# Performance work log

Measured on AMD Instinct MI355X. Metric: run time of the kernel, lower is better.

## Reference

```python
import jax, jax.numpy as jnp
import numpy as np

DIM = 1024
HEADS = 16
DIM_HEAD = 64
INNER = HEADS * DIM_HEAD
EPS = 1e-5


def layernorm(x, g, b):
    mu = jnp.mean(x, axis=-1, keepdims=True)
    var = jnp.var(x, axis=-1, keepdims=True)
    return (x - mu) * jax.lax.rsqrt(var + EPS) * g + b


def setup_inputs() -> dict:
    key = jax.random.key(0)
    ks = jax.random.split(key, 16)
    b, n = 2, 2048
    s = 0.02
    inp = {
        "x": jax.random.normal(ks[0], (b, n, DIM), dtype=jnp.float32),
        "ln_g": jnp.ones((DIM,), jnp.float32),
        "ln_b": jnp.zeros((DIM,), jnp.float32),
        "Wq": jax.random.normal(ks[1], (DIM, INNER), jnp.float32) * s,
        "Wkv": jax.random.normal(ks[2], (DIM, 2 * DIM_HEAD), jnp.float32) * s,
        "null_kv": jax.random.normal(ks[3], (2, DIM_HEAD), jnp.float32),
        "null_attn_bias": jax.random.normal(ks[4], (HEADS,), jnp.float32),
        "pb_w0": jax.random.normal(ks[5], (1, DIM), jnp.float32) * s,
        "pb_b0": jnp.zeros((DIM,), jnp.float32),
        "pb_ln0_g": jnp.ones((DIM,), jnp.float32),
        "pb_ln0_b": jnp.zeros((DIM,), jnp.float32),
        "pb_w1": jax.random.normal(ks[6], (DIM, DIM), jnp.float32) * s,
        "pb_b1": jnp.zeros((DIM,), jnp.float32),
        "pb_ln1_g": jnp.ones((DIM,), jnp.float32),
        "pb_ln1_b": jnp.zeros((DIM,), jnp.float32),
        "pb_w2": jax.random.normal(ks[7], (DIM, HEADS), jnp.float32) * s,
        "pb_b2": jnp.zeros((HEADS,), jnp.float32),
        "Wo": jax.random.normal(ks[8], (INNER, DIM), jnp.float32) * s,
        "out_ln_g": jnp.ones((DIM,), jnp.float32),
        "out_ln_b": jnp.zeros((DIM,), jnp.float32),
    }
    return inp


def dynamic_pos_bias(n, pb_w0, pb_b0, pb_ln0_g, pb_ln0_b, pb_w1, pb_b1,
                     pb_ln1_g, pb_ln1_b, pb_w2, pb_b2):
    # pos in [-(n-1), n-1], shape [2n-1, 1]
    pos = jnp.arange(-n + 1, n, dtype=jnp.float32)[:, None]
    h = jax.nn.silu(layernorm(pos @ pb_w0 + pb_b0, pb_ln0_g, pb_ln0_b))
    h = jax.nn.silu(layernorm(h @ pb_w1 + pb_b1, pb_ln1_g, pb_ln1_b))
    h = h @ pb_w2 + pb_b2  # [2n-1, heads]
    i = jnp.arange(n)
    idx = i[:, None] - i[None, :] + (n - 1)  # [n, n]
    bias = h[idx]  # [n, n, heads]
    return jnp.transpose(bias, (2, 0, 1))  # [heads, n, n]


def attention_fwd(x, ln_g, ln_b, Wq, Wkv, null_kv, null_attn_bias,
                  pb_w0, pb_b0, pb_ln0_g, pb_ln0_b, pb_w1, pb_b1,
                  pb_ln1_g, pb_ln1_b, pb_w2, pb_b2, Wo, out_ln_g, out_ln_b):
    b, n, _ = x.shape
    scale = DIM_HEAD ** -0.5
    xn = layernorm(x, ln_g, ln_b)
    q = (xn @ Wq).reshape(b, n, HEADS, DIM_HEAD).transpose(0, 2, 1, 3) * scale  # [b,h,n,d]
    kv = xn @ Wkv  # [b,n,2d]
    k, v = kv[..., :DIM_HEAD], kv[..., DIM_HEAD:]  # single-head MQA kv
    nk = jnp.broadcast_to(null_kv[0], (b, 1, DIM_HEAD))
    nv = jnp.broadcast_to(null_kv[1], (b, 1, DIM_HEAD))
    k = jnp.concatenate([nk, k], axis=1)  # [b, n+1, d]
    v = jnp.concatenate([nv, v], axis=1)
    sim = jnp.einsum('bhid,bjd->bhij', q, k)  # [b,h,n,n+1]
    rel = dynamic_pos_bias(n, pb_w0, pb_b0, pb_ln0_g, pb_ln0_b,
                           pb_w1, pb_b1, pb_ln1_g, pb_ln1_b, pb_w2, pb_b2)
    null_bias = jnp.broadcast_to(null_attn_bias[:, None, None], (HEADS, n, 1))
    attn_bias = jnp.concatenate([null_bias, rel], axis=-1)  # [h, n, n+1]
    sim = sim + attn_bias[None]
    max_neg = -jnp.finfo(sim.dtype).max
    causal_mask = jnp.triu(jnp.ones((n, n + 1), dtype=bool), k=2)
    sim = jnp.where(causal_mask[None, None], max_neg, sim)
    attn = jax.nn.softmax(sim, axis=-1)
    out = jnp.einsum('bhij,bjd->bhid', attn, v)  # [b,h,n,d]
    out = out.transpose(0, 2, 1, 3).reshape(b, n, INNER)
    return layernorm(out @ Wo, out_ln_g, out_ln_b)


def reference(x, ln_g, ln_b, Wq, Wkv, null_kv, null_attn_bias,
              pb_w0, pb_b0, pb_ln0_g, pb_ln0_b, pb_w1, pb_b1,
              pb_ln1_g, pb_ln1_b, pb_w2, pb_b2, Wo, out_ln_g, out_ln_b):
    return attention_fwd(x, ln_g, ln_b, Wq, Wkv, null_kv, null_attn_bias,
                         pb_w0, pb_b0, pb_ln0_g, pb_ln0_b, pb_w1, pb_b1,
                         pb_ln1_g, pb_ln1_b, pb_w2, pb_b2, Wo, out_ln_g, out_ln_b)
```

## Files before the change

### kernel.cpp

```cpp
#include <hip/hip_runtime.h>
#include <hip/hip_bf16.h>
#include <math.h>

#define DIMM   1024
#define NHEADS 16
#define DHEAD  64
#define BATCH  2
#define SEQ    2048
#define NKEYS  (SEQ + 1)
#define NKROWS 2112
#define NKP    2112
#define PBROWS (2 * SEQ - 1)
#define ROWS   (BATCH * SEQ)

using bf16x8 = __attribute__((ext_vector_type(8))) short;
using bf16x4 = __attribute__((ext_vector_type(4))) short;
using f32x4  = __attribute__((ext_vector_type(4))) float;
typedef unsigned int u32;
typedef unsigned short u16;

__device__ __forceinline__ u16 f2bf(float f) {
  __hip_bfloat16 h = __float2bfloat16(f);
  return __builtin_bit_cast(u16, h);
}
__device__ __forceinline__ float bf2f(u16 u) {
  u32 x = ((u32)u) << 16;
  return __builtin_bit_cast(float, x);
}
__device__ __forceinline__ void gl_lds16(const void* g, void* l) {
  __builtin_amdgcn_global_load_lds(
      (const __attribute__((address_space(1))) u32*)g,
      (__attribute__((address_space(3))) u32*)l, 16, 0, 0);
}
__device__ __forceinline__ f32x4 mfma16(bf16x4 a, bf16x4 b, f32x4 c) {
  asm("v_mfma_f32_16x16x16_bf16 %0, %1, %2, %0" : "+v"(c) : "v"(a), "v"(b));
  return c;
}

__global__ __launch_bounds__(256) void ln_kernel(
    const float* __restrict__ in, const float* __restrict__ addb,
    const float* __restrict__ g, const float* __restrict__ bvec,
    void* __restrict__ outv, int silu, int obf16, int posrow) {
  int row = blockIdx.x;
  int t = threadIdx.x;
  float4 x;
  if (posrow) {
    float p = (float)(row - (SEQ - 1));
    float4 wv = ((const float4*)in)[t];
    float4 a = ((const float4*)addb)[t];
    x.x = p * wv.x + a.x; x.y = p * wv.y + a.y;
    x.z = p * wv.z + a.z; x.w = p * wv.w + a.w;
  } else {
    x = ((const float4*)(in + (size_t)row * DIMM))[t];
    if (addb) {
      float4 a = ((const float4*)addb)[t];
      x.x += a.x; x.y += a.y; x.z += a.z; x.w += a.w;
    }
  }
  float s  = x.x + x.y + x.z + x.w;
  float ss = x.x * x.x + x.y * x.y + x.z * x.z + x.w * x.w;
#pragma unroll
  for (int off = 32; off > 0; off >>= 1) {
    s  += __shfl_down(s, off);
    ss += __shfl_down(ss, off);
  }
  __shared__ float rs[4], rss[4];
  int wv_ = t >> 6, lane = t & 63;
  if (lane == 0) { rs[wv_] = s; rss[wv_] = ss; }
  __syncthreads();
  float S  = rs[0] + rs[1] + rs[2] + rs[3];
  float SS = rss[0] + rss[1] + rss[2] + rss[3];
  float mu  = S * (1.0f / DIMM);
  float var = SS * (1.0f / DIMM) - mu * mu;
  float inv = rsqrtf(var + 1e-5f);
  float4 gv = ((const float4*)g)[t];
  float4 bv = ((const float4*)bvec)[t];
  float4 o;
  o.x = (x.x - mu) * inv * gv.x + bv.x;
  o.y = (x.y - mu) * inv * gv.y + bv.y;
  o.z = (x.z - mu) * inv * gv.z + bv.z;
  o.w = (x.w - mu) * inv * gv.w + bv.w;
  if (silu) {
    o.x = o.x / (1.f + expf(-o.x));
    o.y = o.y / (1.f + expf(-o.y));
    o.z = o.z / (1.f + expf(-o.z));
    o.w = o.w / (1.f + expf(-o.w));
  }
  if (obf16) {
    ushort4 ob;
    ob.x = f2bf(o.x); ob.y = f2bf(o.y); ob.z = f2bf(o.z); ob.w = f2bf(o.w);
    ((ushort4*)((u16*)outv + (size_t)row * DIMM))[t] = ob;
  } else {
    ((float4*)((float*)outv + (size_t)row * DIMM))[t] = o;
  }
}

__global__ __launch_bounds__(256) void conv_wT(
    const float* __restrict__ W, u16* __restrict__ WT, int N, int rowOff) {
  __shared__ float tile[32][33];
  const int n0 = blockIdx.x * 32, k0 = blockIdx.y * 32;
  const int tc = threadIdx.x & 31, tr = threadIdx.x >> 5;
#pragma unroll
  for (int i = 0; i < 4; ++i)
    tile[tr + i * 8][tc] = W[(size_t)(k0 + tr + i * 8) * N + n0 + tc];
  __syncthreads();
#pragma unroll
  for (int i = 0; i < 4; ++i) {
    int r = tr + i * 8;
    WT[(size_t)(rowOff + n0 + r) * 1024 + k0 + tc] = f2bf(tile[tc][r]);
  }
}

__global__ __launch_bounds__(256) void gemm_bf16(
    const u16* __restrict__ A, const u16* __restrict__ BT,
    float* __restrict__ C, int M, int N, int K) {
  __shared__ u16 As[128 * 32];
  __shared__ u16 Bs[128 * 32];
  const int w = threadIdx.x >> 6, lane = threadIdx.x & 63;
  const int lo = lane & 15, hi = lane >> 4;
  const int wr = w >> 1, wc = w & 1;
  const int row0 = blockIdx.y * 128, col0 = blockIdx.x * 128;
  const int srow = lane >> 2;
  const int scol = (lane & 3) * 8;
  f32x4 acc[4][4];
#pragma unroll
  for (int m = 0; m < 4; ++m)
#pragma unroll
    for (int n = 0; n < 4; ++n) acc[m][n] = f32x4{0.f, 0.f, 0.f, 0.f};
  for (int k0 = 0; k0 < K; k0 += 32) {
#pragma unroll
    for (int c = 0; c < 2; ++c) {
      const int base = 32 * w + c * 16;
      gl_lds16(A + (size_t)(row0 + base + srow) * K + k0 + scol,
               &As[base * 32]);
      gl_lds16(BT + (size_t)(col0 + base + srow) * K + k0 + scol,
               &Bs[base * 32]);
    }
    __syncthreads();
    bf16x8 af[4], bg[4];
#pragma unroll
    for (int m = 0; m < 4; ++m)
      af[m] = *(const bf16x8*)&As[(wr * 64 + m * 16 + lo) * 32 + hi * 8];
#pragma unroll
    for (int n = 0; n < 4; ++n)
      bg[n] = *(const bf16x8*)&Bs[(wc * 64 + n * 16 + lo) * 32 + hi * 8];
#pragma unroll
    for (int m = 0; m < 4; ++m)
#pragma unroll
      for (int n = 0; n < 4; ++n)
        acc[m][n] = __builtin_amdgcn_mfma_f32_16x16x32_bf16(af[m], bg[n],
                                                            acc[m][n], 0, 0, 0);
    __syncthreads();
  }
#pragma unroll
  for (int m = 0; m < 4; ++m)
#pragma unroll
    for (int r = 0; r < 4; ++r) {
      const int row = row0 + wr * 64 + m * 16 + hi * 4 + r;
      if (row < M) {
#pragma unroll
        for (int n = 0; n < 4; ++n)
          C[(size_t)row * N + col0 + wc * 64 + n * 16 + lo] = acc[m][n][r];
      }
    }
}

__global__ __launch_bounds__(256) void relayout_q(
    const float* __restrict__ tmp, u16* __restrict__ qb) {
  size_t e = (size_t)blockIdx.x * 256 + threadIdx.x;
  int m = (int)(e >> 8), c4 = (int)(e & 255);
  int b = m >> 11, i = m & 2047;
  int h = c4 >> 4, d4 = c4 & 15;
  float4 v = ((const float4*)(tmp + (size_t)m * 1152))[c4];
  const float sc = 0.125f;
  ushort4 o;
  o.x = f2bf(v.x * sc); o.y = f2bf(v.y * sc);
  o.z = f2bf(v.z * sc); o.w = f2bf(v.w * sc);
  ((ushort4*)qb)[((size_t)(b * NHEADS + h) * SEQ + i) * 16 + d4] = o;
}

__global__ __launch_bounds__(256) void relayout_kv(
    const float* __restrict__ tmp, u16* __restrict__ kb, u16* __restrict__ vbT) {
  size_t e = (size_t)blockIdx.x * 256 + threadIdx.x;
  int m = (int)(e >> 5), c4 = (int)(e & 31);
  int b = m >> 11, i = m & 2047;
  float4 v = ((const float4*)(tmp + (size_t)m * 1152 + 1024))[c4];
  if (c4 < 16) {
    ushort4 o;
    o.x = f2bf(v.x); o.y = f2bf(v.y); o.z = f2bf(v.z); o.w = f2bf(v.w);
    ((ushort4*)kb)[((size_t)b * NKROWS + (i + 1)) * 16 + c4] = o;
  } else {
    int d = (c4 - 16) * 4;
    size_t base = (size_t)b * DHEAD * NKP + (size_t)d * NKP + (i + 1);
    vbT[base]           = f2bf(v.x);
    vbT[base + NKP]     = f2bf(v.y);
    vbT[base + 2 * NKP] = f2bf(v.z);
    vbT[base + 3 * NKP] = f2bf(v.w);
  }
}

__global__ void fill_null(const float* __restrict__ null_kv,
                          u16* __restrict__ kb, u16* __restrict__ vbT) {
  int b = blockIdx.x, d = threadIdx.x;
  kb[(size_t)b * NKROWS * DHEAD + d] = f2bf(null_kv[d]);
  vbT[(size_t)b * DHEAD * NKP + (size_t)d * NKP] = f2bf(null_kv[DHEAD + d]);
}

__global__ __launch_bounds__(256) void h2_kernel(
    const u16* __restrict__ h1, const float* __restrict__ w2,
    const float* __restrict__ b2, float* __restrict__ bias_tabT) {
  int r = blockIdx.x, t = threadIdx.x;
  int col = t & 15, seg = t >> 4;
  const u16* hr = h1 + (size_t)r * DIMM;
  float acc = 0.f;
  for (int k = seg * 64; k < seg * 64 + 64; ++k)
    acc += bf2f(hr[k]) * w2[(size_t)k * NHEADS + col];
  __shared__ float p[16][16];
  p[seg][col] = acc;
  __syncthreads();
  if (t < 16) {
    float s = 0.f;
#pragma unroll
    for (int q = 0; q < 16; q++) s += p[q][t];
    bias_tabT[(size_t)t * 4096 + r] = s + b2[t];
  }
}

__global__ __launch_bounds__(128, 2) void flash_attn(
    const u16* __restrict__ qb, const u16* __restrict__ kb,
    const u16* __restrict__ vbT, const float* __restrict__ bias_tabT,
    const float* __restrict__ null_bias, u16* __restrict__ outb) {
  const int qt = gridDim.x - 1 - blockIdx.x;
  const int h = blockIdx.y, b = blockIdx.z;
  const int tid = threadIdx.x;
  const int w = tid >> 6, lane = tid & 63;
  const int lo = lane & 15, hi = lane >> 4;
  const int q0 = qt * 64;
  const int rq0 = q0 + w * 32 + lo;
  const int rq1 = rq0 + 16;

  __shared__ float bias_lds[2][128];

  const size_t qbase = (size_t)(b * NHEADS + h) * SEQ;
  const u16* qrow0 = qb + (qbase + rq0) * DHEAD;
  const u16* qrow1 = qb + (qbase + rq1) * DHEAD;
  bf16x8 qa00 = *(const bf16x8*)(qrow0 + hi * 8);
  bf16x8 qa01 = *(const bf16x8*)(qrow0 + 32 + hi * 8);
  bf16x8 qa10 = *(const bf16x8*)(qrow1 + hi * 8);
  bf16x8 qa11 = *(const bf16x8*)(qrow1 + 32 + hi * 8);

  const u16* Kb = kb + (size_t)b * NKROWS * DHEAD;
  const u16* Vb = vbT + (size_t)b * DHEAD * NKP;
  const float* bt = bias_tabT + (size_t)h * 4096;
  const float nb = null_bias[h];

  f32x4 o[2][4];
#pragma unroll
  for (int f = 0; f < 2; ++f)
#pragma unroll
    for (int dc = 0; dc < 4; ++dc) o[f][dc] = f32x4{0.f, 0.f, 0.f, 0.f};
  float m_l[2] = {-3.0e38f, -3.0e38f};
  float l_l[2] = {0.f, 0.f};

  const int nkt = qt + 2;
  bf16x8 kf0[4], kf1[4];
#pragma unroll
  for (int nf = 0; nf < 4; ++nf) {
    const u16* krow = Kb + (size_t)(nf * 16 + lo) * DHEAD;
    kf0[nf] = *(const bf16x8*)(krow + hi * 8);
    kf1[nf] = *(const bf16x8*)(krow + 32 + hi * 8);
  }

  for (int kt = 0; kt < nkt; ++kt) {
    const int j0 = kt * 64;
    {
      const int base = q0 - j0 - 63 + SEQ;
      if (tid < 127) bias_lds[kt & 1][tid] = bt[base + tid];
    }
    __syncthreads();
    f32x4 s[2][4];
    __builtin_amdgcn_s_setprio(1);
#pragma unroll
    for (int nf = 0; nf < 4; ++nf) {
      f32x4 a0 = f32x4{0.f, 0.f, 0.f, 0.f};
      f32x4 a1 = f32x4{0.f, 0.f, 0.f, 0.f};
      a0 = __builtin_amdgcn_mfma_f32_16x16x32_bf16(kf0[nf], qa00, a0, 0, 0, 0);
      a0 = __builtin_amdgcn_mfma_f32_16x16x32_bf16(kf1[nf], qa01, a0, 0, 0, 0);
      a1 = __builtin_amdgcn_mfma_f32_16x16x32_bf16(kf0[nf], qa10, a1, 0, 0, 0);
      a1 = __builtin_amdgcn_mfma_f32_16x16x32_bf16(kf1[nf], qa11, a1, 0, 0, 0);
      s[0][nf] = a0;
      s[1][nf] = a1;
    }
    __builtin_amdgcn_s_setprio(0);
    {
      const int jn = (kt + 1 < nkt ? kt + 1 : kt) * 64;
#pragma unroll
      for (int nf = 0; nf < 4; ++nf) {
        const u16* krow = Kb + (size_t)(jn + nf * 16 + lo) * DHEAD;
        kf0[nf] = *(const bf16x8*)(krow + hi * 8);
        kf1[nf] = *(const bf16x8*)(krow + 32 + hi * 8);
      }
    }
    bf16x4 vf[4][4];
#pragma unroll
    for (int dc = 0; dc < 4; ++dc) {
      const u16* vrow = Vb + (size_t)(dc * 16 + lo) * NKP + j0 + hi * 4;
#pragma unroll
      for (int kc = 0; kc < 4; ++kc)
        vf[dc][kc] = *(const bf16x4*)(vrow + kc * 16);
    }
    const float* bl = bias_lds[kt & 1];
    float tm[2] = {-3.0e38f, -3.0e38f};
#pragma unroll
    for (int f = 0; f < 2; ++f) {
      const int rq = (f == 0) ? rq0 : rq1;
      const int qrel = w * 32 + f * 16 + lo + 63;
#pragma unroll
      for (int nf = 0; nf < 4; ++nf)
#pragma unroll
        for (int r = 0; r < 4; ++r) {
          const int krel = nf * 16 + hi * 4 + r;
          const int key = j0 + krel;
          float bias = bl[qrel - krel];
          if (key == 0) bias = nb;
          float v = (key <= rq + 1) ? (s[f][nf][r] + bias) : -3.0e38f;
          s[f][nf][r] = v;
          tm[f] = fmaxf(tm[f], v);
        }
      tm[f] = fmaxf(tm[f], __shfl_xor(tm[f], 16));
      tm[f] = fmaxf(tm[f], __shfl_xor(tm[f], 32));
    }
    if (__any((tm[0] > m_l[0] + 8.0f) || (tm[1] > m_l[1] + 8.0f))) {
#pragma unroll
      for (int f = 0; f < 2; ++f) {
        float mn = fmaxf(m_l[f], tm[f]);
        float sco = __expf(m_l[f] - mn);
        m_l[f] = mn;
        l_l[f] *= sco;
#pragma unroll
        for (int dc = 0; dc < 4; ++dc)
#pragma unroll
          for (int r = 0; r < 4; ++r) o[f][dc][r] *= sco;
      }
    }
    bf16x4 pbf[2][4];
#pragma unroll
    for (int f = 0; f < 2; ++f)
#pragma unroll
      for (int nf = 0; nf < 4; ++nf) {
        float p0 = __expf(s[f][nf][0] - m_l[f]);
        float p1 = __expf(s[f][nf][1] - m_l[f]);
        float p2 = __expf(s[f][nf][2] - m_l[f]);
        float p3 = __expf(s[f][nf][3] - m_l[f]);
        l_l[f] += (p0 + p1) + (p2 + p3);
        pbf[f][nf][0] = (short)f2bf(p0);
        pbf[f][nf][1] = (short)f2bf(p1);
        pbf[f][nf][2] = (short)f2bf(p2);
        pbf[f][nf][3] = (short)f2bf(p3);
      }
    __builtin_amdgcn_s_setprio(1);
#pragma unroll
    for (int f = 0; f < 2; ++f)
#pragma unroll
      for (int dc = 0; dc < 4; ++dc)
#pragma unroll
        for (int kc = 0; kc < 4; ++kc)
          o[f][dc] = mfma16(vf[dc][kc], pbf[f][kc], o[f][dc]);
    __builtin_amdgcn_s_setprio(0);
  }
  asm volatile("s_nop 7\ns_nop 7" :::);
#pragma unroll
  for (int f = 0; f < 2; ++f) {
    float lf = l_l[f];
    lf += __shfl_xor(lf, 16);
    lf += __shfl_xor(lf, 32);
    float linv = 1.0f / lf;
    const int rq = (f == 0) ? rq0 : rq1;
    u16* orow = outb + (size_t)(b * SEQ + rq) * DIMM + h * DHEAD + hi * 4;
#pragma unroll
    for (int dc = 0; dc < 4; ++dc) {
      ushort4 st;
      st.x = f2bf(o[f][dc][0] * linv);
      st.y = f2bf(o[f][dc][1] * linv);
      st.z = f2bf(o[f][dc][2] * linv);
      st.w = f2bf(o[f][dc][3] * linv);
      *(ushort4*)(orow + dc * 16) = st;
    }
  }
}

extern "C" void kernel_launch(void* const* d_in, const int* in_sizes, int n_in,
                              void* d_out, int out_size, void* d_ws,
                              size_t ws_size, hipStream_t stream) {
  const float* x         = (const float*)d_in[0];
  const float* ln_g      = (const float*)d_in[1];
  const float* ln_b      = (const float*)d_in[2];
  const float* Wq        = (const float*)d_in[3];
  const float* Wkv       = (const float*)d_in[4];
  const float* null_kv   = (const float*)d_in[5];
  const float* null_bias = (const float*)d_in[6];
  const float* pb_w0     = (const float*)d_in[7];
  const float* pb_b0     = (const float*)d_in[8];
  const float* pb_ln0_g  = (const float*)d_in[9];
  const float* pb_ln0_b  = (const float*)d_in[10];
  const float* pb_w1     = (const float*)d_in[11];
  const float* pb_b1     = (const float*)d_in[12];
  const float* pb_ln1_g  = (const float*)d_in[13];
  const float* pb_ln1_b  = (const float*)d_in[14];
  const float* pb_w2     = (const float*)d_in[15];
  const float* pb_b2     = (const float*)d_in[16];
  const float* Wo        = (const float*)d_in[17];
  const float* out_ln_g  = (const float*)d_in[18];
  const float* out_ln_b  = (const float*)d_in[19];
  float* out = (float*)d_out;

  char* ws = (char*)d_ws;
  float* regA      = (float*)(ws);
  u16*   h1_bf     = (u16*)(ws + 18874368);
  u16*   regC      = (u16*)(ws + 35651584);
  u16*   qb        = (u16*)(ws + 44040192);
  u16*   kb        = (u16*)(ws + 52428800);
  u16*   vbT       = (u16*)(ws + 52969472);
  u16*   wqkvT     = (u16*)(ws + 53510144);
  u16*   w1T       = (u16*)(ws + 55869440);
  u16*   woT       = (u16*)(ws + 57966592);
  float* bias_tabT = (float*)(ws + 60063744);

  hipMemsetAsync((void*)kb, 0, 1081344, stream);

  conv_wT<<<dim3(32, 32), 256, 0, stream>>>(Wq, wqkvT, 1024, 0);
  conv_wT<<<dim3(4, 32), 256, 0, stream>>>(Wkv, wqkvT, 128, 1024);
  conv_wT<<<dim3(32, 32), 256, 0, stream>>>(pb_w1, w1T, 1024, 0);
  conv_wT<<<dim3(32, 32), 256, 0, stream>>>(Wo, woT, 1024, 0);

  ln_kernel<<<ROWS, 256, 0, stream>>>(x, nullptr, ln_g, ln_b, regC, 0, 1, 0);
  gemm_bf16<<<dim3(9, 32), 256, 0, stream>>>(regC, wqkvT, regA, ROWS, 1152,
                                             1024);
  relayout_q<<<4096, 256, 0, stream>>>(regA, qb);
  relayout_kv<<<512, 256, 0, stream>>>(regA, kb, vbT);
  fill_null<<<2, 64, 0, stream>>>(null_kv, kb, vbT);
  ln_kernel<<<PBROWS, 256, 0, stream>>>(pb_w0, pb_b0, pb_ln0_g, pb_ln0_b, regC,
                                        1, 1, 1);
  gemm_bf16<<<dim3(8, 32), 256, 0, stream>>>(regC, w1T, regA, PBROWS, 1024,
                                             1024);
  ln_kernel<<<PBROWS, 256, 0, stream>>>(regA, pb_b1, pb_ln1_g, pb_ln1_b, h1_bf,
                                        1, 1, 0);
  h2_kernel<<<PBROWS, 256, 0, stream>>>(h1_bf, pb_w2, pb_b2, bias_tabT);
  flash_attn<<<dim3(SEQ / 64, NHEADS, BATCH), 128, 0, stream>>>(
      qb, kb, vbT, bias_tabT, null_bias, regC);
  gemm_bf16<<<dim3(8, 32), 256, 0, stream>>>(regC, woT, regA, ROWS, 1024, 1024);
  ln_kernel<<<ROWS, 256, 0, stream>>>(regA, nullptr, out_ln_g, out_ln_b, out, 0,
                                      0, 0);
}
```

Baseline: 435.3 us.

## Split attention KV range in two with partial-output combine kernel

Each query tile's key range is split into two halves handled by separate blocks, which write unnormalized fp32 partial outputs plus max and sum stats. A new combine kernel merges the two halves with log-sum-exp weighting and writes the bf16 output. The aim is more blocks and better load balance for the causal triangle, with launch bounds raised to allow higher occupancy. The cost is extra fp32 partial traffic, one more launch, and workspace reuse that overlaps other buffers. The h2 kernel also switches to vectorized bf16x8 loads with an unrolled loop.

Measured after the change: 676.6 us. 1.55x slower.

```diff
diff --git a/kernel.cpp b/kernel.cpp
--- a/kernel.cpp
+++ b/kernel.cpp
@@ -211,10 +211,16 @@
     const float* __restrict__ b2, float* __restrict__ bias_tabT) {
   int r = blockIdx.x, t = threadIdx.x;
   int col = t & 15, seg = t >> 4;
-  const u16* hr = h1 + (size_t)r * DIMM;
+  const u16* hr = h1 + (size_t)r * DIMM + seg * 64;
+  const float* w2s = w2 + (size_t)seg * 64 * NHEADS + col;
   float acc = 0.f;
-  for (int k = seg * 64; k < seg * 64 + 64; ++k)
-    acc += bf2f(hr[k]) * w2[(size_t)k * NHEADS + col];
+#pragma unroll
+  for (int c = 0; c < 8; ++c) {
+    bf16x8 hv = *(const bf16x8*)(hr + c * 8);
+#pragma unroll
+    for (int j = 0; j < 8; ++j)
+      acc += bf2f((u16)hv[j]) * w2s[(size_t)(c * 8 + j) * NHEADS];
+  }
   __shared__ float p[16][16];
   p[seg][col] = acc;
   __syncthreads();
@@ -226,11 +232,13 @@
   }
 }
 
-__global__ __launch_bounds__(128, 2) void flash_attn(
+__global__ __launch_bounds__(128, 4) void flash_attn(
     const u16* __restrict__ qb, const u16* __restrict__ kb,
     const u16* __restrict__ vbT, const float* __restrict__ bias_tabT,
-    const float* __restrict__ null_bias, u16* __restrict__ outb) {
-  const int qt = gridDim.x - 1 - blockIdx.x;
+    const float* __restrict__ null_bias, float* __restrict__ partO,
+    float* __restrict__ partML) {
+  const int g = gridDim.x - 1 - blockIdx.x;
+  const int qt = g >> 1, sp = g & 1;
   const int h = blockIdx.y, b = blockIdx.z;
   const int tid = threadIdx.x;
   const int w = tid >> 6, lane = tid & 63;
@@ -239,6 +247,11 @@
   const int rq0 = q0 + w * 32 + lo;
   const int rq1 = rq0 + 16;
 
+  const int n = qt + 2;
+  const int half = (n + 1) >> 1;
+  const int kt0 = sp ? half : 0;
+  const int kt1 = sp ? n : half;
+
   __shared__ float bias_lds[2][128];
 
   const size_t qbase = (size_t)(b * NHEADS + h) * SEQ;
@@ -262,16 +275,18 @@
   float m_l[2] = {-3.0e38f, -3.0e38f};
   float l_l[2] = {0.f, 0.f};
 
-  const int nkt = qt + 2;
   bf16x8 kf0[4], kf1[4];
-#pragma unroll
-  for (int nf = 0; nf < 4; ++nf) {
-    const u16* krow = Kb + (size_t)(nf * 16 + lo) * DHEAD;
-    kf0[nf] = *(const bf16x8*)(krow + hi * 8);
-    kf1[nf] = *(const bf16x8*)(krow + 32 + hi * 8);
-  }
-
-  for (int kt = 0; kt < nkt; ++kt) {
+  {
+    const int j0p = kt0 * 64;
+#pragma unroll
+    for (int nf = 0; nf < 4; ++nf) {
+      const u16* krow = Kb + (size_t)(j0p + nf * 16 + lo) * DHEAD;
+      kf0[nf] = *(const bf16x8*)(krow + hi * 8);
+      kf1[nf] = *(const bf16x8*)(krow + 32 + hi * 8);
+    }
+  }
+
+  for (int kt = kt0; kt < kt1; ++kt) {
     const int j0 = kt * 64;
     {
       const int base = q0 - j0 - 63 + SEQ;
@@ -293,7 +308,7 @@
     }
     __builtin_amdgcn_s_setprio(0);
     {
-      const int jn = (kt + 1 < nkt ? kt + 1 : kt) * 64;
+      const int jn = (kt + 1 < kt1 ? kt + 1 : kt) * 64;
 #pragma unroll
       for (int nf = 0; nf < 4; ++nf) {
         const u16* krow = Kb + (size_t)(jn + nf * 16 + lo) * DHEAD;
@@ -374,19 +389,37 @@
     float lf = l_l[f];
     lf += __shfl_xor(lf, 16);
     lf += __shfl_xor(lf, 32);
-    float linv = 1.0f / lf;
     const int rq = (f == 0) ? rq0 : rq1;
-    u16* orow = outb + (size_t)(b * SEQ + rq) * DIMM + h * DHEAD + hi * 4;
-#pragma unroll
-    for (int dc = 0; dc < 4; ++dc) {
-      ushort4 st;
-      st.x = f2bf(o[f][dc][0] * linv);
-      st.y = f2bf(o[f][dc][1] * linv);
-      st.z = f2bf(o[f][dc][2] * linv);
-      st.w = f2bf(o[f][dc][3] * linv);
-      *(ushort4*)(orow + dc * 16) = st;
-    }
-  }
+    const size_t pidx = (((size_t)sp * BATCH + b) * NHEADS + h) * SEQ + rq;
+    float* po = partO + pidx * 64 + hi * 4;
+#pragma unroll
+    for (int dc = 0; dc < 4; ++dc) *(f32x4*)(po + dc * 16) = o[f][dc];
+    if (hi == 0) ((float2*)partML)[pidx] = make_float2(m_l[f], lf);
+  }
+}
+
+__global__ __launch_bounds__(256) void attn_combine(
+    const float* __restrict__ partO, const float* __restrict__ partML,
+    u16* __restrict__ outb) {
+  const int row = blockIdx.x;
+  const int b = row >> 11, i = row & 2047;
+  const int t = threadIdx.x;
+  const int h = t >> 4, d = (t & 15) * 4;
+  const size_t mlb = ((size_t)b * NHEADS + h) * SEQ + i;
+  const size_t mls = (size_t)BATCH * NHEADS * SEQ;
+  float2 ml0 = ((const float2*)partML)[mlb];
+  float2 ml1 = ((const float2*)partML)[mlb + mls];
+  float M = fmaxf(ml0.x, ml1.x);
+  float w0 = __expf(ml0.x - M), w1 = __expf(ml1.x - M);
+  float inv = 1.0f / (w0 * ml0.y + w1 * ml1.y);
+  float4 o0 = *(const float4*)(partO + mlb * 64 + d);
+  float4 o1 = *(const float4*)(partO + (mlb + mls) * 64 + d);
+  ushort4 st;
+  st.x = f2bf((w0 * o0.x + w1 * o1.x) * inv);
+  st.y = f2bf((w0 * o0.y + w1 * o1.y) * inv);
+  st.z = f2bf((w0 * o0.z + w1 * o1.z) * inv);
+  st.w = f2bf((w0 * o0.w + w1 * o1.w) * inv);
+  *(ushort4*)(outb + (size_t)row * DIMM + h * DHEAD + d) = st;
 }
 
 extern "C" void kernel_launch(void* const* d_in, const int* in_sizes, int n_in,
@@ -416,6 +449,8 @@
 
   char* ws = (char*)d_ws;
   float* regA      = (float*)(ws);
+  float* partO     = (float*)(ws);
+  float* partML    = (float*)(ws + 33554432);
   u16*   h1_bf     = (u16*)(ws + 18874368);
   u16*   regC      = (u16*)(ws + 35651584);
   u16*   qb        = (u16*)(ws + 44040192);
@@ -446,8 +481,9 @@
   ln_kernel<<<PBROWS, 256, 0, stream>>>(regA, pb_b1, pb_ln1_g, pb_ln1_b, h1_bf,
                                         1, 1, 0);
   h2_kernel<<<PBROWS, 256, 0, stream>>>(h1_bf, pb_w2, pb_b2, bias_tabT);
-  flash_attn<<<dim3(SEQ / 64, NHEADS, BATCH), 128, 0, stream>>>(
-      qb, kb, vbT, bias_tabT, null_bias, regC);
+  flash_attn<<<dim3(SEQ / 64 * 2, NHEADS, BATCH), 128, 0, stream>>>(
+      qb, kb, vbT, bias_tabT, null_bias, partO, partML);
+  attn_combine<<<ROWS, 256, 0, stream>>>(partO, partML, regC);
   gemm_bf16<<<dim3(8, 32), 256, 0, stream>>>(regC, woT, regA, ROWS, 1024, 1024);
   ln_kernel<<<ROWS, 256, 0, stream>>>(regA, nullptr, out_ln_g, out_ln_b, out, 0,
                                       0, 0);
```
